# Performance work log

Measured on AMD Instinct MI355X. Metric: run time of the kernel, lower is better.

## Reference

```python
import jax, jax.numpy as jnp
import numpy as np

B, H, W = 64, 512, 512
HS = (3, 3)  # h_shape


def setup_inputs() -> dict:
    key = jax.random.key(0)
    k1, k2 = jax.random.split(key)
    x = jax.random.normal(k1, (B, H, W), dtype=jnp.float32)
    # filter param: fixed 1.0 at [0,0], small trainable values elsewhere
    w = 0.01 * jax.random.normal(k2, HS, dtype=jnp.float32)
    w = w.at[0, 0].set(1.0)
    return {"x": x, "w": w}


def reference(x, w):
    # pad input by H/4, W/4 on each side of the last two dims
    ph, pw = x.shape[-2] // 4, x.shape[-1] // 4
    xm = jnp.pad(x, ((0, 0), (ph, ph), (pw, pw)))
    Hp, Wp = xm.shape[-2], xm.shape[-1]
    # zero-pad small filter to the padded grid (top-left corner)
    hm1 = jnp.pad(w, ((0, Hp - w.shape[-2]), (0, Wp - w.shape[-1])))
    # frequency-domain reciprocal filter, shape [Hp, Wp//2+1]
    gm1f = 1.0 / jnp.fft.rfft2(hm1)
    gm2f = jnp.roll(gm1f[::-1, :], shift=1, axis=0)
    gm3f = jnp.roll(gm1f[:, ::-1], shift=1, axis=1)
    gm4f = jnp.roll(gm3f[::-1, :], shift=1, axis=0)
    gmf = (gm1f * gm2f) * (gm3f * gm4f)
    # apply in frequency domain and invert
    ymf = gmf[None, :, :] * jnp.fft.rfft2(xm)
    ym = jnp.fft.irfft2(ymf, s=(Hp, Wp))
    return ym
```

## Files before the change

### kernel.cpp

```cpp
#include <hip/hip_runtime.h>

#define HP   768
#define NV   385
#define HIN  512
#define WIN  512
#define K    8
#define A    17
#define PADO 136
#define TW   64
#define TH   64
#define LH   80
#define LWL  80
#define LWS  84
#define HROWS 40
#define HSIZE (HROWS * LWS)

#define OB   120
#define OE   648
#define NT9  9
#define ACT0_Q 30
#define ACT1_Q 174

#define TWO_PI_OVER_HP 0.008181230868723419f

typedef float f4v __attribute__((ext_vector_type(4)));

__device__ inline float2 cmul(float2 a, float2 b) {
    return make_float2(a.x*b.x - a.y*b.y, a.x*b.y + a.y*b.x);
}

__device__ inline float2 evalF_t(int u, int v, const float* w9,
                                 const float2* __restrict__ tbl) {
    float fr = 0.f, fi = 0.f;
#pragma unroll
    for (int i = 0; i < 3; ++i) {
#pragma unroll
        for (int j = 0; j < 3; ++j) {
            int idx = u * i + v * j;
            if (idx >= 2 * HP) idx -= 2 * HP;
            if (idx >= HP)     idx -= HP;
            float2 e = tbl[idx];
            float wv = w9[i * 3 + j];
            fr += wv * e.x;
            fi -= wv * e.y;
        }
    }
    return make_float2(fr, fi);
}

__global__ __launch_bounds__(320) void filt_P_kernel(
        const float* __restrict__ w, float2* __restrict__ P) {
    __shared__ float2 tbl[HP];
    __shared__ float2 lg[HP];
    __shared__ float2 red[20][16];
    int v = blockIdx.x;
    int tid = threadIdx.x;

    float w9[9];
#pragma unroll
    for (int i = 0; i < 9; ++i) w9[i] = w[i];

    for (int m = tid; m < HP; m += 320) {
        float s, c;
        sincosf((float)m * TWO_PI_OVER_HP, &s, &c);
        tbl[m] = make_float2(c, s);
    }
    __syncthreads();

    int sv = (v == 0) ? 0 : (NV - v);
    for (int u = tid; u < HP; u += 320) {
        int su = (HP - u) % HP;
        float2 F1 = evalF_t(u,  v,  w9, tbl);
        float2 F2 = evalF_t(su, v,  w9, tbl);
        float2 F3 = evalF_t(u,  sv, w9, tbl);
        float2 F4 = evalF_t(su, sv, w9, tbl);
        float2 pr = cmul(cmul(F1, F2), cmul(F3, F4));
        float d = pr.x * pr.x + pr.y * pr.y;
        lg[u] = make_float2(pr.x / d, -pr.y / d);
    }
    __syncthreads();

    int a   = tid >> 4;
    int sub = tid & 15;
    if (a < A) {
        int ap  = a - K;
        int apu = (ap < 0) ? ap + HP : ap;
        float Pr = 0.f, Pi = 0.f;
        for (int u = sub; u < HP; u += 16) {
            int idx = (u * apu) % HP;
            float2 e = tbl[idx];
            float2 g = lg[u];
            Pr += g.x * e.x - g.y * e.y;
            Pi += g.x * e.y + g.y * e.x;
        }
        red[a][sub] = make_float2(Pr, Pi);
    }
    __syncthreads();
    if (tid < A) {
        float Pr = 0.f, Pi = 0.f;
#pragma unroll
        for (int s2 = 0; s2 < 16; ++s2) { Pr += red[tid][s2].x; Pi += red[tid][s2].y; }
        P[tid * NV + v] = make_float2(Pr, Pi);
    }
}

__global__ __launch_bounds__(256) void filt_gk_kernel(
        const float2* __restrict__ P, float* __restrict__ gkf) {
    __shared__ float2 tbl[HP];
    int tid = threadIdx.x;
    int id = blockIdx.x * 256 + tid;
    for (int m = tid; m < HP; m += 256) {
        float s, c;
        sincosf((float)m * TWO_PI_OVER_HP, &s, &c);
        tbl[m] = make_float2(c, s);
    }
    __syncthreads();
    if (id >= A * A) return;
    int ai = id / A;
    int bi = id - ai * A;
    int bp = bi - K;
    int bpu = (bp < 0) ? bp + HP : bp;
    float sum = 0.f;
    int idx = 0;
    for (int vv = 0; vv < NV; ++vv) {
        float wv = (vv == 0 || vv == NV - 1) ? 1.f : 2.f;
        float2 e = tbl[idx];
        float2 p = P[ai * NV + vv];
        sum += wv * (p.x * e.x - p.y * e.y);
        idx += bpu;
        if (idx >= HP) idx -= HP;
    }
    gkf[(2 * K - ai) * A + (2 * K - bi)] = sum * (1.f / ((float)HP * (float)HP));
}

__global__ __launch_bounds__(256) void zero_border_kernel(float* __restrict__ out) {
    int gid  = blockIdx.x;
    int img  = gid / 192;
    int rg   = gid - img * 192;
    int lane = threadIdx.x & 63;
    int w    = threadIdx.x >> 6;
    int row  = rg * 4 + w;
    f4v* base = (f4v*)(out + ((size_t)img * HP + row) * HP);
    f4v z = {0.f, 0.f, 0.f, 0.f};
    if (row >= OB && row < OB + NT9 * TH) {
        if (lane < ACT0_Q)
            __builtin_nontemporal_store(z, base + lane);
        else if (lane < ACT0_Q + (192 - ACT1_Q))
            __builtin_nontemporal_store(z, base + ACT1_Q + (lane - ACT0_Q));
    } else {
        __builtin_nontemporal_store(z, base + lane);
        __builtin_nontemporal_store(z, base + lane + 64);
        __builtin_nontemporal_store(z, base + lane + 128);
    }
}

__global__ __launch_bounds__(256, 4) void deconv_kernel(
        const float* __restrict__ x, const float* __restrict__ gkf,
        float* __restrict__ out) {
    __shared__ __align__(16) float tile[2 * HSIZE];

    const int tx = threadIdx.x;
    const int ty = threadIdx.y;
    const int tid = ty * 8 + tx;
    const int bx = blockIdx.x, by = blockIdx.y, bz = blockIdx.z;

    const int ix0 = bx * TW + (OB - PADO);
    const int iy0 = by * TH + (OB - PADO);
    const int oy0 = OB + by * TH + ty * 2;
    const int ox0 = OB + bx * TW + tx * 8;
    float* orow0 = out + ((size_t)bz * HP + oy0) * HP + ox0;
    float* orow1 = orow0 + HP;

    const float* xb = x + (size_t)bz * (HIN * WIN);
    for (int l = tid; l < LH * (LWL / 4); l += 256) {
        int r = l / 20, c4 = l - r * 20;
        int gy = iy0 + r;
        int gx = ix0 + c4 * 4;
        float4 val = make_float4(0.f, 0.f, 0.f, 0.f);
        if ((unsigned)gy < (unsigned)HIN && (unsigned)gx < (unsigned)WIN)
            val = *(const float4*)&xb[gy * WIN + gx];
        *(float4*)&tile[(r & 1) * HSIZE + (r >> 1) * LWS + c4 * 4] = val;
    }
    __syncthreads();

    if (oy0 >= OE) {
        f4v z = {0.f, 0.f, 0.f, 0.f};
        __builtin_nontemporal_store(z, (f4v*)orow0);
        __builtin_nontemporal_store(z, (f4v*)orow0 + 1);
        __builtin_nontemporal_store(z, (f4v*)orow1);
        __builtin_nontemporal_store(z, (f4v*)orow1 + 1);
        return;
    }

    const float* tE = tile;
    const float* tO = tile + HSIZE;

    float accA[8], accB[8];
#pragma unroll
    for (int c = 0; c < 8; ++c) { accA[c] = 0.f; accB[c] = 0.f; }
    float rbA[24], rbB[24];

    auto loadRow = [&](float* rb, const float* tb, int rowp) {
        const float* p = tb + rowp * LWS + tx * 8;
#pragma unroll
        for (int q = 0; q < 6; ++q)
            *(float4*)&rb[q * 4] = *(const float4*)&p[q * 4];
    };
    auto fmaRow = [&](const float* gp, const float* r, float* acc) {
#pragma unroll
        for (int bb = 0; bb < A; ++bb) {
            float g = gp[bb];
#pragma unroll
            for (int c = 0; c < 8; ++c)
                acc[c] += g * r[bb + c];
        }
    };

    loadRow(rbA, tE, ty);
#pragma unroll 1
    for (int aa = 0; aa < 16; aa += 2) {
        int h = aa >> 1;
        loadRow(rbB, tO, ty + h);
        fmaRow(gkf + aa * A, rbA, accA);
        fmaRow(gkf + aa * A, rbB, accB);
        loadRow(rbA, tE, ty + h + 1);
        fmaRow(gkf + (aa + 1) * A, rbB, accA);
        fmaRow(gkf + (aa + 1) * A, rbA, accB);
    }
    loadRow(rbB, tO, ty + 8);
    fmaRow(gkf + 16 * A, rbA, accA);
    fmaRow(gkf + 16 * A, rbB, accB);

    f4v vA0 = {accA[0], accA[1], accA[2], accA[3]};
    f4v vA1 = {accA[4], accA[5], accA[6], accA[7]};
    f4v vB0 = {accB[0], accB[1], accB[2], accB[3]};
    f4v vB1 = {accB[4], accB[5], accB[6], accB[7]};
    __builtin_nontemporal_store(vA0, (f4v*)orow0);
    __builtin_nontemporal_store(vA1, (f4v*)orow0 + 1);
    __builtin_nontemporal_store(vB0, (f4v*)orow1);
    __builtin_nontemporal_store(vB1, (f4v*)orow1 + 1);
}

extern "C" void kernel_launch(void* const* d_in, const int* in_sizes, int n_in,
                              void* d_out, int out_size, void* d_ws, size_t ws_size,
                              hipStream_t stream) {
    const float* x = (const float*)d_in[0];
    const float* w = (const float*)d_in[1];
    float* out = (float*)d_out;

    float2* P   = (float2*)d_ws;
    float*  gkf = (float*)d_ws + (size_t)A * NV * 2;

    filt_P_kernel<<<dim3(NV), dim3(320), 0, stream>>>(w, P);
    filt_gk_kernel<<<dim3(2), dim3(256), 0, stream>>>(P, gkf);
    zero_border_kernel<<<dim3(64 * 192), dim3(256), 0, stream>>>(out);
    deconv_kernel<<<dim3(NT9, NT9, 64), dim3(8, 32), 0, stream>>>(x, gkf, out);
}
```

Before: 380.8 us.

## Parallelize filter-kernel reduction across 17 blocks and raise deconv occupancy hint

The 17x17 spatial filter computation previously ran on two blocks, with each thread doing a serial 385-step loop over global P. It now launches one block per filter row. Each block stages its P row in shared memory and splits the sum across 16 lanes, then reduces through shared memory. Separately, the deconv kernel's launch bounds ask for 6 waves per SIMD instead of 4, which may force register spilling in the heavily unrolled FMA loop.

```diff
diff --git a/kernel.cpp b/kernel.cpp
--- a/kernel.cpp
+++ b/kernel.cpp
@@ -104,33 +104,45 @@
     }
 }
 
-__global__ __launch_bounds__(256) void filt_gk_kernel(
+__global__ __launch_bounds__(320) void filt_gk_kernel(
         const float2* __restrict__ P, float* __restrict__ gkf) {
     __shared__ float2 tbl[HP];
+    __shared__ float2 Prow[NV];
+    __shared__ float  red[20][16];
+    int ai  = blockIdx.x;
     int tid = threadIdx.x;
-    int id = blockIdx.x * 256 + tid;
-    for (int m = tid; m < HP; m += 256) {
+
+    for (int m = tid; m < HP; m += 320) {
         float s, c;
         sincosf((float)m * TWO_PI_OVER_HP, &s, &c);
         tbl[m] = make_float2(c, s);
     }
-    __syncthreads();
-    if (id >= A * A) return;
-    int ai = id / A;
-    int bi = id - ai * A;
-    int bp = bi - K;
-    int bpu = (bp < 0) ? bp + HP : bp;
-    float sum = 0.f;
-    int idx = 0;
-    for (int vv = 0; vv < NV; ++vv) {
-        float wv = (vv == 0 || vv == NV - 1) ? 1.f : 2.f;
-        float2 e = tbl[idx];
-        float2 p = P[ai * NV + vv];
-        sum += wv * (p.x * e.x - p.y * e.y);
-        idx += bpu;
-        if (idx >= HP) idx -= HP;
-    }
-    gkf[(2 * K - ai) * A + (2 * K - bi)] = sum * (1.f / ((float)HP * (float)HP));
+    for (int m = tid; m < NV; m += 320)
+        Prow[m] = P[ai * NV + m];
+    __syncthreads();
+
+    int bi  = tid >> 4;
+    int sub = tid & 15;
+    if (bi < A) {
+        int bp  = bi - K;
+        int bpu = (bp < 0) ? bp + HP : bp;
+        float sum = 0.f;
+        for (int vv = sub; vv < NV; vv += 16) {
+            float wv = (vv == 0 || vv == NV - 1) ? 1.f : 2.f;
+            int idx = (vv * bpu) % HP;
+            float2 e = tbl[idx];
+            float2 p = Prow[vv];
+            sum += wv * (p.x * e.x - p.y * e.y);
+        }
+        red[bi][sub] = sum;
+    }
+    __syncthreads();
+    if (tid < A) {
+        float s = 0.f;
+#pragma unroll
+        for (int s2 = 0; s2 < 16; ++s2) s += red[tid][s2];
+        gkf[(2 * K - ai) * A + (2 * K - tid)] = s * (1.f / ((float)HP * (float)HP));
+    }
 }
 
 __global__ __launch_bounds__(256) void zero_border_kernel(float* __restrict__ out) {
@@ -154,7 +166,7 @@
     }
 }
 
-__global__ __launch_bounds__(256, 4) void deconv_kernel(
+__global__ __launch_bounds__(256, 6) void deconv_kernel(
         const float* __restrict__ x, const float* __restrict__ gkf,
         float* __restrict__ out) {
     __shared__ __align__(16) float tile[2 * HSIZE];
@@ -252,7 +264,7 @@
     float*  gkf = (float*)d_ws + (size_t)A * NV * 2;
 
     filt_P_kernel<<<dim3(NV), dim3(320), 0, stream>>>(w, P);
-    filt_gk_kernel<<<dim3(2), dim3(256), 0, stream>>>(P, gkf);
+    filt_gk_kernel<<<dim3(A), dim3(320), 0, stream>>>(P, gkf);
     zero_border_kernel<<<dim3(64 * 192), dim3(256), 0, stream>>>(out);
     deconv_kernel<<<dim3(NT9, NT9, 64), dim3(8, 32), 0, stream>>>(x, gkf, out);
 }
```

Measured after the change: 317.3 us. 16.7% less time.
